# Optimization experiments

Hardware: AMD Instinct MI355X
Metric: run time of the kernel (lower is better)

## Reference

```python
import jax, jax.numpy as jnp
import numpy as np

D_MODEL = 1024
N_HEADS = 16
D_K = D_MODEL // N_HEADS
BATCH = 2
SEQ = 2048


def setup_inputs() -> dict:
    key = jax.random.key(0)
    ks = jax.random.split(key, 6)
    scale = 1.0 / np.sqrt(D_MODEL)
    x = jax.random.normal(ks[0], (BATCH, SEQ, D_MODEL), dtype=jnp.float32)
    position_bias = jax.random.normal(ks[1], (N_HEADS, SEQ, SEQ), dtype=jnp.float32)
    w_q = jax.random.normal(ks[2], (D_MODEL, D_MODEL), dtype=jnp.float32) * scale
    w_k = jax.random.normal(ks[3], (D_MODEL, D_MODEL), dtype=jnp.float32) * scale
    w_v = jax.random.normal(ks[4], (D_MODEL, D_MODEL), dtype=jnp.float32) * scale
    w_o = jax.random.normal(ks[5], (D_MODEL, D_MODEL), dtype=jnp.float32) * scale
    return {"x": x, "position_bias": position_bias, "w_q": w_q, "w_k": w_k, "w_v": w_v, "w_o": w_o}


def reference(x, position_bias, w_q, w_k, w_v, w_o):
    B, n, _ = x.shape
    # Linear(d,d,bias=False): y = x @ W^T
    def split_heads(t):
        return t.reshape(B, n, N_HEADS, D_K).transpose(0, 2, 1, 3)  # [B,H,n,d_k]
    Q = split_heads(x @ w_q.T)
    K = split_heads(x @ w_k.T)
    V = split_heads(x @ w_v.T)
    # T5-style: no 1/sqrt(d_k) scaling
    scores = jnp.einsum('bhqd,bhkd->bhqk', Q, K) + position_bias[None]
    attn = jax.nn.softmax(scores.astype(jnp.float32), axis=-1).astype(scores.dtype)
    ctx = jnp.einsum('bhqk,bhkd->bhqd', attn, V)  # [B,H,n,d_k]
    attention = ctx.transpose(0, 2, 1, 3).reshape(B, n, D_MODEL)
    return attention @ w_o.T
```

## Files before the change

### kernel.cpp

```cpp
#include <hip/hip_runtime.h>


typedef _Float16 f16_t;
typedef _Float16 f16x8 __attribute__((ext_vector_type(8)));
typedef _Float16 f16x4 __attribute__((ext_vector_type(4)));
typedef float   floatx4 __attribute__((ext_vector_type(4)));

#define MFMA16(a, b, c) __builtin_amdgcn_mfma_f32_16x16x32_f16((a), (b), (c), 0, 0, 0)

__global__ __launch_bounds__(256) void cvt_f32_f16(const float* __restrict__ src,
                                                   f16_t* __restrict__ dst, int n) {
  int i = (blockIdx.x * 256 + threadIdx.x) * 4;
  if (i < n) {
    floatx4 v = *(const floatx4*)(src + i);
    f16x4 o;
    o.x = (_Float16)v.x; o.y = (_Float16)v.y; o.z = (_Float16)v.z; o.w = (_Float16)v.w;
    *(f16x4*)(dst + i) = o;
  }
}

__global__ __launch_bounds__(256) void qkv_gemm(
    const f16_t* __restrict__ xb,
    const f16_t* __restrict__ wqb, const f16_t* __restrict__ wkb,
    const f16_t* __restrict__ wvb,
    f16_t* __restrict__ qb, f16_t* __restrict__ kb, f16_t* __restrict__ vb) {
  __shared__ f16_t As[64][72];
  __shared__ f16_t Bs[64][72];
  const int t = threadIdx.x;
  const int w = t >> 6, lane = t & 63, quad = lane >> 4, col = lane & 15;
  const int mbase = blockIdx.x * 64;
  const int nt = blockIdx.y;
  const int which = nt >> 4;
  const int ncol0 = (nt & 15) * 64;
  const f16_t* wsel = (which == 0) ? wqb : (which == 1) ? wkb : wvb;
  f16_t* osel = (which == 0) ? qb : (which == 1) ? kb : vb;

  floatx4 zero4 = {0.f, 0.f, 0.f, 0.f};
  floatx4 acc[4];
  acc[0] = acc[1] = acc[2] = acc[3] = zero4;

  for (int kt = 0; kt < 16; ++kt) {
    const int k0 = kt * 64;
#pragma unroll
    for (int rep = 0; rep < 2; ++rep) {
      int cid = t + rep * 256;
      int r = cid >> 3, c = (cid & 7) * 8;
      *(f16x8*)&As[r][c] = *(const f16x8*)(xb + (size_t)(mbase + r) * 1024 + k0 + c);
      *(f16x8*)&Bs[r][c] = *(const f16x8*)(wsel + (size_t)(ncol0 + r) * 1024 + k0 + c);
    }
    __syncthreads();
#pragma unroll
    for (int ch = 0; ch < 2; ++ch) {
      f16x8 a = *(const f16x8*)&As[w * 16 + col][ch * 32 + quad * 8];
#pragma unroll
      for (int cb = 0; cb < 4; ++cb) {
        f16x8 b = *(const f16x8*)&Bs[cb * 16 + col][ch * 32 + quad * 8];
        acc[cb] = MFMA16(a, b, acc[cb]);
      }
    }
    __syncthreads();
  }
#pragma unroll
  for (int cb = 0; cb < 4; ++cb) {
#pragma unroll
    for (int i = 0; i < 4; ++i) {
      int m = mbase + w * 16 + quad * 4 + i;
      int nf = ncol0 + cb * 16 + col;
      int h = nf >> 6, d = nf & 63;
      int bb = m >> 11, s = m & 2047;
      osel[(size_t)(((bb * 16 + h) * 2048) + s) * 64 + d] = (f16_t)acc[cb][i];
    }
  }
}

__global__ __launch_bounds__(256) void out_gemm(
    const f16_t* __restrict__ ab, const f16_t* __restrict__ wob,
    float* __restrict__ outp) {
  __shared__ f16_t As[64][72];
  __shared__ f16_t Bs[64][72];
  const int t = threadIdx.x;
  const int w = t >> 6, lane = t & 63, quad = lane >> 4, col = lane & 15;
  const int mbase = blockIdx.x * 64;
  const int nbase = blockIdx.y * 64;

  floatx4 zero4 = {0.f, 0.f, 0.f, 0.f};
  floatx4 acc[4];
  acc[0] = acc[1] = acc[2] = acc[3] = zero4;

  for (int kt = 0; kt < 16; ++kt) {
    const int k0 = kt * 64;
#pragma unroll
    for (int rep = 0; rep < 2; ++rep) {
      int cid = t + rep * 256;
      int r = cid >> 3, c = (cid & 7) * 8;
      *(f16x8*)&As[r][c] = *(const f16x8*)(ab + (size_t)(mbase + r) * 1024 + k0 + c);
      *(f16x8*)&Bs[r][c] = *(const f16x8*)(wob + (size_t)(nbase + r) * 1024 + k0 + c);
    }
    __syncthreads();
#pragma unroll
    for (int ch = 0; ch < 2; ++ch) {
      f16x8 a = *(const f16x8*)&As[w * 16 + col][ch * 32 + quad * 8];
#pragma unroll
      for (int cb = 0; cb < 4; ++cb) {
        f16x8 b = *(const f16x8*)&Bs[cb * 16 + col][ch * 32 + quad * 8];
        acc[cb] = MFMA16(a, b, acc[cb]);
      }
    }
    __syncthreads();
  }
#pragma unroll
  for (int cb = 0; cb < 4; ++cb) {
#pragma unroll
    for (int i = 0; i < 4; ++i) {
      int m = mbase + w * 16 + quad * 4 + i;
      int n = nbase + cb * 16 + col;
      outp[(size_t)m * 1024 + n] = acc[cb][i];
    }
  }
}

__global__ __launch_bounds__(512) void attn_kernel(
    const f16_t* __restrict__ qb, const f16_t* __restrict__ kb,
    const f16_t* __restrict__ vb, const float* __restrict__ bias,
    f16_t* __restrict__ ctxb) {
  __shared__ f16_t Ks[2][64][72];
  __shared__ f16_t Vt[2][64][72];
  __shared__ f16_t biasS[64][72];
  __shared__ f16_t Ps[8][16][72];

  const int t = threadIdx.x;
  const int w = t >> 6, lane = t & 63, quad = lane >> 4, col = lane & 15;
  const int bb = w >> 2, w4 = w & 3;
  const int h = blockIdx.y;
  const int qbase = blockIdx.x * 64;

  f16x8 qf[2];
  {
    const f16_t* qp = qb + (size_t)(((bb * 16 + h) * 2048) + qbase + w4 * 16 + col) * 64;
    qf[0] = *(const f16x8*)(qp + quad * 8);
    qf[1] = *(const f16x8*)(qp + 32 + quad * 8);
  }

  float mprev[4], lrun[4];
  floatx4 zero4 = {0.f, 0.f, 0.f, 0.f};
  floatx4 oacc[4];
#pragma unroll
  for (int i = 0; i < 4; ++i) { mprev[i] = -3e38f; lrun[i] = 0.f; }
  oacc[0] = oacc[1] = oacc[2] = oacc[3] = zero4;

  for (int kt = 0; kt < 32; ++kt) {
    const int kbase = kt * 64;
#pragma unroll
    for (int rep = 0; rep < 2; ++rep) {
      int cid = t + rep * 512;
      int b2 = cid >> 9, rem = cid & 511;
      int r = rem >> 3, c = (rem & 7) * 8;
      *(f16x8*)&Ks[b2][r][c] =
          *(const f16x8*)(kb + (size_t)(((b2 * 16 + h) * 2048) + kbase + r) * 64 + c);
    }
    if (t < 256) {
      int b2 = t >> 7, rem = t & 127;
      int kk0 = (rem & 15) * 4, d0 = (rem >> 4) * 8;
      f16x8 rows[4];
#pragma unroll
      for (int j = 0; j < 4; ++j)
        rows[j] = *(const f16x8*)(vb +
            (size_t)(((b2 * 16 + h) * 2048) + kbase + kk0 + j) * 64 + d0);
#pragma unroll
      for (int d = 0; d < 8; ++d) {
        f16x4 pk;
        pk.x = rows[0][d]; pk.y = rows[1][d]; pk.z = rows[2][d]; pk.w = rows[3][d];
        *(f16x4*)&Vt[b2][d0 + d][kk0] = pk;
      }
    }
    {
      int r = t >> 3, c0 = (t & 7) * 8;
      const float* bp = bias + ((size_t)h * 2048 + qbase + r) * 2048 + kbase + c0;
      floatx4 v0 = *(const floatx4*)bp;
      floatx4 v1 = *(const floatx4*)(bp + 4);
      f16x8 bo;
      bo[0] = (_Float16)v0.x; bo[1] = (_Float16)v0.y;
      bo[2] = (_Float16)v0.z; bo[3] = (_Float16)v0.w;
      bo[4] = (_Float16)v1.x; bo[5] = (_Float16)v1.y;
      bo[6] = (_Float16)v1.z; bo[7] = (_Float16)v1.w;
      *(f16x8*)&biasS[r][c0] = bo;
    }
    __syncthreads();

    floatx4 sacc[4];
    sacc[0] = sacc[1] = sacc[2] = sacc[3] = zero4;
#pragma unroll
    for (int ch = 0; ch < 2; ++ch) {
#pragma unroll
      for (int cb = 0; cb < 4; ++cb) {
        f16x8 kf = *(const f16x8*)&Ks[bb][cb * 16 + col][ch * 32 + quad * 8];
        sacc[cb] = MFMA16(qf[ch], kf, sacc[cb]);
      }
    }
    float sv[4][4];
#pragma unroll
    for (int cb = 0; cb < 4; ++cb)
#pragma unroll
      for (int i = 0; i < 4; ++i)
        sv[cb][i] = sacc[cb][i] +
                    (float)biasS[w4 * 16 + quad * 4 + i][cb * 16 + col];

    float alpha[4];
#pragma unroll
    for (int i = 0; i < 4; ++i) {
      float rm = fmaxf(fmaxf(sv[0][i], sv[1][i]), fmaxf(sv[2][i], sv[3][i]));
#pragma unroll
      for (int msk = 1; msk < 16; msk <<= 1)
        rm = fmaxf(rm, __shfl_xor(rm, msk, 64));
      float mnew = fmaxf(mprev[i], rm);
      alpha[i] = __expf(mprev[i] - mnew);
      float rs = 0.f;
#pragma unroll
      for (int cb = 0; cb < 4; ++cb) {
        float p = __expf(sv[cb][i] - mnew);
        sv[cb][i] = p;
        rs += p;
      }
#pragma unroll
      for (int msk = 1; msk < 16; msk <<= 1)
        rs += __shfl_xor(rs, msk, 64);
      lrun[i] = lrun[i] * alpha[i] + rs;
      mprev[i] = mnew;
    }
#pragma unroll
    for (int cb = 0; cb < 4; ++cb)
#pragma unroll
      for (int i = 0; i < 4; ++i)
        Ps[w][quad * 4 + i][cb * 16 + col] = (f16_t)sv[cb][i];
#pragma unroll
    for (int db = 0; db < 4; ++db) {
      oacc[db].x *= alpha[0]; oacc[db].y *= alpha[1];
      oacc[db].z *= alpha[2]; oacc[db].w *= alpha[3];
    }
#pragma unroll
    for (int ch = 0; ch < 2; ++ch) {
      f16x8 pf = *(const f16x8*)&Ps[w][col][ch * 32 + quad * 8];
#pragma unroll
      for (int db = 0; db < 4; ++db) {
        f16x8 vf = *(const f16x8*)&Vt[bb][db * 16 + col][ch * 32 + quad * 8];
        oacc[db] = MFMA16(pf, vf, oacc[db]);
      }
    }
    __syncthreads();
  }

#pragma unroll
  for (int db = 0; db < 4; ++db)
#pragma unroll
    for (int i = 0; i < 4; ++i) {
      int m = bb * 2048 + qbase + w4 * 16 + quad * 4 + i;
      int n = h * 64 + db * 16 + col;
      ctxb[(size_t)m * 1024 + n] = (f16_t)(oacc[db][i] / lrun[i]);
    }
}

extern "C" void kernel_launch(void* const* d_in, const int* in_sizes, int n_in,
                              void* d_out, int out_size, void* d_ws, size_t ws_size,
                              hipStream_t stream) {
  const float* x    = (const float*)d_in[0];
  const float* bias = (const float*)d_in[1];
  const float* wq   = (const float*)d_in[2];
  const float* wk   = (const float*)d_in[3];
  const float* wv   = (const float*)d_in[4];
  const float* wo   = (const float*)d_in[5];
  float* outp = (float*)d_out;
  char* ws = (char*)d_ws;
  const size_t MB = 1u << 20;

  f16_t* xb   = (f16_t*)(ws);
  f16_t* wqb  = (f16_t*)(ws + 8 * MB);
  f16_t* wkb  = (f16_t*)(ws + 10 * MB);
  f16_t* wvb  = (f16_t*)(ws + 12 * MB);
  f16_t* wob  = (f16_t*)(ws + 14 * MB);
  f16_t* qb   = (f16_t*)(ws + 16 * MB);
  f16_t* kb   = (f16_t*)(ws + 24 * MB);
  f16_t* vb   = (f16_t*)(ws + 32 * MB);
  f16_t* ctxb = (f16_t*)(ws + 40 * MB);

  cvt_f32_f16<<<4096, 256, 0, stream>>>(x, xb, 4194304);
  cvt_f32_f16<<<1024, 256, 0, stream>>>(wq, wqb, 1048576);
  cvt_f32_f16<<<1024, 256, 0, stream>>>(wk, wkb, 1048576);
  cvt_f32_f16<<<1024, 256, 0, stream>>>(wv, wvb, 1048576);
  cvt_f32_f16<<<1024, 256, 0, stream>>>(wo, wob, 1048576);

  qkv_gemm<<<dim3(64, 48), 256, 0, stream>>>(xb, wqb, wkb, wvb, qb, kb, vb);
  attn_kernel<<<dim3(32, 16), 512, 0, stream>>>(qb, kb, vb, bias, ctxb);
  out_gemm<<<dim3(64, 16), 256, 0, stream>>>(ctxb, wob, outp);
}
```

Before: 543.4 us.

## Enlarge GEMM tiles to 128x128 and keep attention probabilities in registers

Both projection GEMMs move from 64x64 tiles with one 16-row strip per wave to 128x128 tiles where each wave computes a 4x4 grid of MFMA blocks, raising operand reuse from LDS and cutting the number of blocks. The attention kernel computes S transposed (K as the A operand), so each lane holds one query column. That lets the softmax row reductions drop from 4-step to 2-step shuffles, and P can be fed directly from registers into 16x16x16 MFMAs without the Ps LDS round-trip. The risks are higher register pressure in the GEMMs and fewer blocks, 256 for out_gemm, which could underfill the GPU's compute units.

```diff
diff --git a/kernel.cpp b/kernel.cpp
--- a/kernel.cpp
+++ b/kernel.cpp
@@ -6,7 +6,8 @@
 typedef _Float16 f16x4 __attribute__((ext_vector_type(4)));
 typedef float   floatx4 __attribute__((ext_vector_type(4)));
 
-#define MFMA16(a, b, c) __builtin_amdgcn_mfma_f32_16x16x32_f16((a), (b), (c), 0, 0, 0)
+#define MFMA16(a, b, c)    __builtin_amdgcn_mfma_f32_16x16x32_f16((a), (b), (c), 0, 0, 0)
+#define MFMA16K16(a, b, c) __builtin_amdgcn_mfma_f32_16x16x16f16((a), (b), (c), 0, 0, 0)
 
 __global__ __launch_bounds__(256) void cvt_f32_f16(const float* __restrict__ src,
                                                    f16_t* __restrict__ dst, int n) {
@@ -24,25 +25,28 @@
     const f16_t* __restrict__ wqb, const f16_t* __restrict__ wkb,
     const f16_t* __restrict__ wvb,
     f16_t* __restrict__ qb, f16_t* __restrict__ kb, f16_t* __restrict__ vb) {
-  __shared__ f16_t As[64][72];
-  __shared__ f16_t Bs[64][72];
+  __shared__ f16_t As[128][72];
+  __shared__ f16_t Bs[128][72];
   const int t = threadIdx.x;
   const int w = t >> 6, lane = t & 63, quad = lane >> 4, col = lane & 15;
-  const int mbase = blockIdx.x * 64;
-  const int nt = blockIdx.y;
-  const int which = nt >> 4;
-  const int ncol0 = (nt & 15) * 64;
+  const int wm = w & 1, wn = w >> 1;
+  const int mbase = blockIdx.x * 128;
+  const int which = blockIdx.y >> 3;
+  const int ncol0 = (blockIdx.y & 7) * 128;
   const f16_t* wsel = (which == 0) ? wqb : (which == 1) ? wkb : wvb;
   f16_t* osel = (which == 0) ? qb : (which == 1) ? kb : vb;
 
   floatx4 zero4 = {0.f, 0.f, 0.f, 0.f};
-  floatx4 acc[4];
-  acc[0] = acc[1] = acc[2] = acc[3] = zero4;
+  floatx4 acc[4][4];
+#pragma unroll
+  for (int i = 0; i < 4; ++i)
+#pragma unroll
+    for (int j = 0; j < 4; ++j) acc[i][j] = zero4;
 
   for (int kt = 0; kt < 16; ++kt) {
     const int k0 = kt * 64;
 #pragma unroll
-    for (int rep = 0; rep < 2; ++rep) {
+    for (int rep = 0; rep < 4; ++rep) {
       int cid = t + rep * 256;
       int r = cid >> 3, c = (cid & 7) * 8;
       *(f16x8*)&As[r][c] = *(const f16x8*)(xb + (size_t)(mbase + r) * 1024 + k0 + c);
@@ -51,46 +55,57 @@
     __syncthreads();
 #pragma unroll
     for (int ch = 0; ch < 2; ++ch) {
-      f16x8 a = *(const f16x8*)&As[w * 16 + col][ch * 32 + quad * 8];
-#pragma unroll
-      for (int cb = 0; cb < 4; ++cb) {
-        f16x8 b = *(const f16x8*)&Bs[cb * 16 + col][ch * 32 + quad * 8];
-        acc[cb] = MFMA16(a, b, acc[cb]);
-      }
-    }
-    __syncthreads();
-  }
-#pragma unroll
-  for (int cb = 0; cb < 4; ++cb) {
-#pragma unroll
-    for (int i = 0; i < 4; ++i) {
-      int m = mbase + w * 16 + quad * 4 + i;
-      int nf = ncol0 + cb * 16 + col;
-      int h = nf >> 6, d = nf & 63;
-      int bb = m >> 11, s = m & 2047;
-      osel[(size_t)(((bb * 16 + h) * 2048) + s) * 64 + d] = (f16_t)acc[cb][i];
-    }
-  }
+      f16x8 a[4], b[4];
+#pragma unroll
+      for (int i = 0; i < 4; ++i)
+        a[i] = *(const f16x8*)&As[wm * 64 + i * 16 + col][ch * 32 + quad * 8];
+#pragma unroll
+      for (int j = 0; j < 4; ++j)
+        b[j] = *(const f16x8*)&Bs[wn * 64 + j * 16 + col][ch * 32 + quad * 8];
+#pragma unroll
+      for (int i = 0; i < 4; ++i)
+#pragma unroll
+        for (int j = 0; j < 4; ++j)
+          acc[i][j] = MFMA16(a[i], b[j], acc[i][j]);
+    }
+    __syncthreads();
+  }
+#pragma unroll
+  for (int i = 0; i < 4; ++i)
+#pragma unroll
+    for (int j = 0; j < 4; ++j)
+#pragma unroll
+      for (int rr = 0; rr < 4; ++rr) {
+        int m = mbase + wm * 64 + i * 16 + quad * 4 + rr;
+        int nf = ncol0 + wn * 64 + j * 16 + col;
+        int h = nf >> 6, d = nf & 63;
+        int bb2 = m >> 11, s = m & 2047;
+        osel[(size_t)(((bb2 * 16 + h) * 2048) + s) * 64 + d] = (f16_t)acc[i][j][rr];
+      }
 }
 
 __global__ __launch_bounds__(256) void out_gemm(
     const f16_t* __restrict__ ab, const f16_t* __restrict__ wob,
     float* __restrict__ outp) {
-  __shared__ f16_t As[64][72];
-  __shared__ f16_t Bs[64][72];
+  __shared__ f16_t As[128][72];
+  __shared__ f16_t Bs[128][72];
   const int t = threadIdx.x;
   const int w = t >> 6, lane = t & 63, quad = lane >> 4, col = lane & 15;
-  const int mbase = blockIdx.x * 64;
-  const int nbase = blockIdx.y * 64;
+  const int wm = w & 1, wn = w >> 1;
+  const int mbase = blockIdx.x * 128;
+  const int nbase = blockIdx.y * 128;
 
   floatx4 zero4 = {0.f, 0.f, 0.f, 0.f};
-  floatx4 acc[4];
-  acc[0] = acc[1] = acc[2] = acc[3] = zero4;
+  floatx4 acc[4][4];
+#pragma unroll
+  for (int i = 0; i < 4; ++i)
+#pragma unroll
+    for (int j = 0; j < 4; ++j) acc[i][j] = zero4;
 
   for (int kt = 0; kt < 16; ++kt) {
     const int k0 = kt * 64;
 #pragma unroll
-    for (int rep = 0; rep < 2; ++rep) {
+    for (int rep = 0; rep < 4; ++rep) {
       int cid = t + rep * 256;
       int r = cid >> 3, c = (cid & 7) * 8;
       *(f16x8*)&As[r][c] = *(const f16x8*)(ab + (size_t)(mbase + r) * 1024 + k0 + c);
@@ -99,24 +114,31 @@
     __syncthreads();
 #pragma unroll
     for (int ch = 0; ch < 2; ++ch) {
-      f16x8 a = *(const f16x8*)&As[w * 16 + col][ch * 32 + quad * 8];
-#pragma unroll
-      for (int cb = 0; cb < 4; ++cb) {
-        f16x8 b = *(const f16x8*)&Bs[cb * 16 + col][ch * 32 + quad * 8];
-        acc[cb] = MFMA16(a, b, acc[cb]);
-      }
-    }
-    __syncthreads();
-  }
-#pragma unroll
-  for (int cb = 0; cb < 4; ++cb) {
-#pragma unroll
-    for (int i = 0; i < 4; ++i) {
-      int m = mbase + w * 16 + quad * 4 + i;
-      int n = nbase + cb * 16 + col;
-      outp[(size_t)m * 1024 + n] = acc[cb][i];
-    }
-  }
+      f16x8 a[4], b[4];
+#pragma unroll
+      for (int i = 0; i < 4; ++i)
+        a[i] = *(const f16x8*)&As[wm * 64 + i * 16 + col][ch * 32 + quad * 8];
+#pragma unroll
+      for (int j = 0; j < 4; ++j)
+        b[j] = *(const f16x8*)&Bs[wn * 64 + j * 16 + col][ch * 32 + quad * 8];
+#pragma unroll
+      for (int i = 0; i < 4; ++i)
+#pragma unroll
+        for (int j = 0; j < 4; ++j)
+          acc[i][j] = MFMA16(a[i], b[j], acc[i][j]);
+    }
+    __syncthreads();
+  }
+#pragma unroll
+  for (int i = 0; i < 4; ++i)
+#pragma unroll
+    for (int j = 0; j < 4; ++j)
+#pragma unroll
+      for (int rr = 0; rr < 4; ++rr) {
+        int m = mbase + wm * 64 + i * 16 + quad * 4 + rr;
+        int n = nbase + wn * 64 + j * 16 + col;
+        outp[(size_t)m * 1024 + n] = acc[i][j][rr];
+      }
 }
 
 __global__ __launch_bounds__(512) void attn_kernel(
@@ -124,9 +146,8 @@
     const f16_t* __restrict__ vb, const float* __restrict__ bias,
     f16_t* __restrict__ ctxb) {
   __shared__ f16_t Ks[2][64][72];
-  __shared__ f16_t Vt[2][64][72];
+  __shared__ f16_t Vt[2][64][76];
   __shared__ f16_t biasS[64][72];
-  __shared__ f16_t Ps[8][16][72];
 
   const int t = threadIdx.x;
   const int w = t >> 6, lane = t & 63, quad = lane >> 4, col = lane & 15;
@@ -141,11 +162,9 @@
     qf[1] = *(const f16x8*)(qp + 32 + quad * 8);
   }
 
-  float mprev[4], lrun[4];
+  float mprev = -3e38f, lrun = 0.f;
   floatx4 zero4 = {0.f, 0.f, 0.f, 0.f};
   floatx4 oacc[4];
-#pragma unroll
-  for (int i = 0; i < 4; ++i) { mprev[i] = -3e38f; lrun[i] = 0.f; }
   oacc[0] = oacc[1] = oacc[2] = oacc[3] = zero4;
 
   for (int kt = 0; kt < 32; ++kt) {
@@ -194,68 +213,73 @@
 #pragma unroll
       for (int cb = 0; cb < 4; ++cb) {
         f16x8 kf = *(const f16x8*)&Ks[bb][cb * 16 + col][ch * 32 + quad * 8];
-        sacc[cb] = MFMA16(qf[ch], kf, sacc[cb]);
+        sacc[cb] = MFMA16(kf, qf[ch], sacc[cb]);
       }
     }
     float sv[4][4];
 #pragma unroll
+    for (int cb = 0; cb < 4; ++cb) {
+      f16x4 b4 = *(const f16x4*)&biasS[w4 * 16 + col][cb * 16 + quad * 4];
+#pragma unroll
+      for (int i = 0; i < 4; ++i)
+        sv[cb][i] = sacc[cb][i] + (float)b4[i];
+    }
+    float rm = -3e38f;
+#pragma unroll
     for (int cb = 0; cb < 4; ++cb)
 #pragma unroll
-      for (int i = 0; i < 4; ++i)
-        sv[cb][i] = sacc[cb][i] +
-                    (float)biasS[w4 * 16 + quad * 4 + i][cb * 16 + col];
-
-    float alpha[4];
-#pragma unroll
-    for (int i = 0; i < 4; ++i) {
-      float rm = fmaxf(fmaxf(sv[0][i], sv[1][i]), fmaxf(sv[2][i], sv[3][i]));
-#pragma unroll
-      for (int msk = 1; msk < 16; msk <<= 1)
-        rm = fmaxf(rm, __shfl_xor(rm, msk, 64));
-      float mnew = fmaxf(mprev[i], rm);
-      alpha[i] = __expf(mprev[i] - mnew);
-      float rs = 0.f;
-#pragma unroll
-      for (int cb = 0; cb < 4; ++cb) {
+      for (int i = 0; i < 4; ++i) rm = fmaxf(rm, sv[cb][i]);
+    rm = fmaxf(rm, __shfl_xor(rm, 16, 64));
+    rm = fmaxf(rm, __shfl_xor(rm, 32, 64));
+    float mnew = fmaxf(mprev, rm);
+    float alpha = __expf(mprev - mnew);
+    mprev = mnew;
+    float ls = 0.f;
+#pragma unroll
+    for (int cb = 0; cb < 4; ++cb)
+#pragma unroll
+      for (int i = 0; i < 4; ++i) {
         float p = __expf(sv[cb][i] - mnew);
         sv[cb][i] = p;
-        rs += p;
-      }
-#pragma unroll
-      for (int msk = 1; msk < 16; msk <<= 1)
-        rs += __shfl_xor(rs, msk, 64);
-      lrun[i] = lrun[i] * alpha[i] + rs;
-      mprev[i] = mnew;
-    }
-#pragma unroll
-    for (int cb = 0; cb < 4; ++cb)
-#pragma unroll
-      for (int i = 0; i < 4; ++i)
-        Ps[w][quad * 4 + i][cb * 16 + col] = (f16_t)sv[cb][i];
+        ls += p;
+      }
+    lrun = lrun * alpha + ls;
+    float a0 = __shfl(alpha, quad * 4 + 0, 64);
+    float a1 = __shfl(alpha, quad * 4 + 1, 64);
+    float a2 = __shfl(alpha, quad * 4 + 2, 64);
+    float a3 = __shfl(alpha, quad * 4 + 3, 64);
 #pragma unroll
     for (int db = 0; db < 4; ++db) {
-      oacc[db].x *= alpha[0]; oacc[db].y *= alpha[1];
-      oacc[db].z *= alpha[2]; oacc[db].w *= alpha[3];
-    }
-#pragma unroll
-    for (int ch = 0; ch < 2; ++ch) {
-      f16x8 pf = *(const f16x8*)&Ps[w][col][ch * 32 + quad * 8];
+      oacc[db].x *= a0; oacc[db].y *= a1; oacc[db].z *= a2; oacc[db].w *= a3;
+    }
+#pragma unroll
+    for (int cb = 0; cb < 4; ++cb) {
+      f16x4 pf;
+      pf[0] = (_Float16)sv[cb][0]; pf[1] = (_Float16)sv[cb][1];
+      pf[2] = (_Float16)sv[cb][2]; pf[3] = (_Float16)sv[cb][3];
 #pragma unroll
       for (int db = 0; db < 4; ++db) {
-        f16x8 vf = *(const f16x8*)&Vt[bb][db * 16 + col][ch * 32 + quad * 8];
-        oacc[db] = MFMA16(pf, vf, oacc[db]);
-      }
-    }
-    __syncthreads();
-  }
-
+        f16x4 vf = *(const f16x4*)&Vt[bb][db * 16 + col][cb * 16 + quad * 4];
+        oacc[db] = MFMA16K16(pf, vf, oacc[db]);
+      }
+    }
+    __syncthreads();
+  }
+
+  float lt = lrun;
+  lt += __shfl_xor(lt, 16, 64);
+  lt += __shfl_xor(lt, 32, 64);
+  float linv[4];
+#pragma unroll
+  for (int i = 0; i < 4; ++i)
+    linv[i] = 1.0f / __shfl(lt, quad * 4 + i, 64);
 #pragma unroll
   for (int db = 0; db < 4; ++db)
 #pragma unroll
     for (int i = 0; i < 4; ++i) {
       int m = bb * 2048 + qbase + w4 * 16 + quad * 4 + i;
       int n = h * 64 + db * 16 + col;
-      ctxb[(size_t)m * 1024 + n] = (f16_t)(oacc[db][i] / lrun[i]);
+      ctxb[(size_t)m * 1024 + n] = (f16_t)(oacc[db][i] * linv[i]);
     }
 }
 
@@ -288,7 +312,7 @@
   cvt_f32_f16<<<1024, 256, 0, stream>>>(wv, wvb, 1048576);
   cvt_f32_f16<<<1024, 256, 0, stream>>>(wo, wob, 1048576);
 
-  qkv_gemm<<<dim3(64, 48), 256, 0, stream>>>(xb, wqb, wkb, wvb, qb, kb, vb);
+  qkv_gemm<<<dim3(32, 24), 256, 0, stream>>>(xb, wqb, wkb, wvb, qb, kb, vb);
   attn_kernel<<<dim3(32, 16), 512, 0, stream>>>(qb, kb, vb, bias, ctxb);
-  out_gemm<<<dim3(64, 16), 256, 0, stream>>>(ctxb, wob, outp);
-}
+  out_gemm<<<dim3(32, 8), 256, 0, stream>>>(ctxb, wob, outp);
+}
```

Measured after the change: 506.8 us. -6.7%, faster.
